# Optimization experiments

Measured on AMD Instinct MI355X. Metric: run time of the kernel, lower is better.

Reference implementation:

```python
import jax, jax.numpy as jnp
import numpy as np

C = 384      # c_s
NF = 16      # n_freq
H = 256      # mlp_hidden
B, K, N = 4, 2048, 16384
POS_WEIGHT = 1.5  # not used; see below


def _ln(x, g, b, eps=1e-5):
    m = x.mean(-1, keepdims=True)
    v = ((x - m) ** 2).mean(-1, keepdims=True)
    return (x - m) * jax.lax.rsqrt(v + eps) * g + b


def setup_inputs() -> dict:
    key = jax.random.key(0)
    ks = jax.random.split(key, 24)
    w = lambda k, shp: (jax.random.normal(k, shp, jnp.float32) * 0.02)
    inp = {
        "s_parent": jax.random.normal(ks[0], (B, K, C), jnp.float32),
        "mu_k": jax.random.normal(ks[1], (B, K, 3), jnp.float32),
        "R_k": jax.random.normal(ks[2], (B, K, 3, 3), jnp.float32),
        "s_k": jax.random.uniform(ks[3], (B, K, 3), jnp.float32),
        "a_idx": jax.random.randint(ks[4], (B, N), 0, K, jnp.int32),
        "node_mask": jnp.ones((B, N), jnp.float32),
        "pos01": jax.random.uniform(ks[5], (B, N), jnp.float32),
        # Pos01FourierEncoder: Linear(2*NF -> C)
        "pos_w": w(ks[6], (C, 2 * NF)), "pos_b": jnp.zeros((C,), jnp.float32),
        # q_proj: LayerNorm(C), Linear(C,C), SiLU, Linear(C,C)
        "q_ln_g": jnp.ones((C,), jnp.float32), "q_ln_b": jnp.zeros((C,), jnp.float32),
        "q_w1": w(ks[7], (C, C)), "q_b1": jnp.zeros((C,), jnp.float32),
        "q_w2": w(ks[8], (C, C)), "q_b2": jnp.zeros((C,), jnp.float32),
        # mlp: LayerNorm(C), Linear(C,H), SiLU, Linear(H,H), SiLU, Linear(H,3)
        "m_ln_g": jnp.ones((C,), jnp.float32), "m_ln_b": jnp.zeros((C,), jnp.float32),
        "m_w1": w(ks[9], (H, C)), "m_b1": jnp.zeros((H,), jnp.float32),
        "m_w2": w(ks[10], (H, H)), "m_b2": jnp.zeros((H,), jnp.float32),
        "m_w3": w(ks[11], (3, H)), "m_b3": jnp.zeros((3,), jnp.float32),
    }
    return inp


def reference(s_parent, mu_k, R_k, s_k, a_idx, node_mask, pos01,
              pos_w, pos_b, q_ln_g, q_ln_b, q_w1, q_b1, q_w2, q_b2,
              m_ln_g, m_ln_b, m_w1, m_b1, m_w2, m_b2, m_w3, m_b3):
    pos_weight = 1.0
    scale = 1.5
    mask = node_mask[..., None]  # [B,N,1]

    # Fourier positional encoding of pos01 in [0,1]
    freqs = (2.0 ** jnp.arange(NF, dtype=jnp.float32)) * np.float32(np.pi)
    ang = pos01[..., None] * freqs                          # [B,N,NF]
    feats = jnp.concatenate([jnp.sin(ang), jnp.cos(ang)], -1)  # [B,N,2NF]
    pos_emb = (feats @ pos_w.T + pos_b) * mask              # [B,N,C]

    idx = jnp.clip(a_idx, 0, K - 1)
    s_pi = jnp.take_along_axis(s_parent, idx[:, :, None], axis=1)  # [B,N,C]
    s_pi = s_pi + pos_weight * pos_emb

    # q_proj
    q = _ln(s_pi, q_ln_g, q_ln_b)
    q = jax.nn.silu(q @ q_w1.T + q_b1)
    q = (q @ q_w2.T + q_b2) * mask

    # mlp -> xi_hat
    h = _ln(q, m_ln_g, m_ln_b)
    h = jax.nn.silu(h @ m_w1.T + m_b1)
    h = jax.nn.silu(h @ m_w2.T + m_b2)
    xi = (h @ m_w3.T + m_b3) * mask
    xi_hat = jnp.tanh(xi) * scale                           # [B,N,3]

    # gather parent rigid params per node
    mu_i = jnp.take_along_axis(mu_k, idx[:, :, None], axis=1)            # [B,N,3]
    s_i = jnp.take_along_axis(jnp.maximum(s_k, 1e-8), idx[:, :, None], axis=1)
    R_i = jnp.take_along_axis(R_k, idx[:, :, None, None], axis=1)        # [B,N,3,3]

    # rigid apply: x = R @ (xi * s) + mu
    x_hat = jnp.einsum('bnij,bnj->bni', R_i, xi_hat * s_i) + mu_i
    x_hat = x_hat * mask
    return xi_hat, x_hat * 10.0, pos01
```

## Files before the change

kernel.cpp:

```cpp
#include <hip/hip_runtime.h>
#include <hip/hip_bf16.h>
#include <math.h>

#define C 384
#define NF 16
#define H 256
#define Bb 4
#define Kk 2048
#define Nn 16384
#define MB 64
#define LDA 392

typedef __attribute__((ext_vector_type(8))) short bf16x8;
typedef __attribute__((ext_vector_type(4))) float f32x4;
typedef __attribute__((ext_vector_type(4))) short s16x4;

#define POS_OFF 0
#define Q1_OFF  12288
#define Q2_OFF  159744
#define M1_OFF  307200
#define M2_OFF  405504
#define M3_OFF  471040
#define W_TOTAL 475136
#define NCONV   ((W_TOTAL + 255) / 256)
#define GQ_OFF 0
#define CQ_OFF 384
#define GM_OFF 768
#define CM_OFF 1024

#define BAR() __asm__ volatile("s_waitcnt lgkmcnt(0)\ns_barrier" ::: "memory")

__device__ __attribute__((always_inline)) inline short f2bf(float x) {
    return __builtin_bit_cast(short, __float2bfloat16(x));
}
__device__ __attribute__((always_inline)) inline float bf2f(short s) {
    return __bfloat162float(__builtin_bit_cast(__hip_bfloat16, s));
}
__device__ __attribute__((always_inline)) inline float silu(float v) {
    return v * __builtin_amdgcn_rcpf(1.f + __expf(-v));
}
__device__ __attribute__((always_inline)) inline s16x4 pack4(f32x4 v) {
    __hip_bfloat162 p0 = __float22bfloat162_rn(float2{v[0], v[1]});
    __hip_bfloat162 p1 = __float22bfloat162_rn(float2{v[2], v[3]});
    s16x4 o;
    o[0] = __builtin_bit_cast(short, p0.x);
    o[1] = __builtin_bit_cast(short, p0.y);
    o[2] = __builtin_bit_cast(short, p1.x);
    o[3] = __builtin_bit_cast(short, p1.y);
    return o;
}

__global__ __launch_bounds__(256) void prep(
    const float* __restrict__ pos_w, const float* __restrict__ q_w1,
    const float* __restrict__ q_w2,  const float* __restrict__ m_w1,
    const float* __restrict__ m_w2,  const float* __restrict__ m_w3,
    const float* __restrict__ q_ln_g, const float* __restrict__ q_ln_b,
    const float* __restrict__ m_ln_g, const float* __restrict__ m_ln_b,
    const float* __restrict__ q_b1,   const float* __restrict__ m_b1,
    short* __restrict__ ws, float* __restrict__ cst)
{
    __shared__ float rg[4], rc[4];
    int tid = threadIdx.x;
    int blk = blockIdx.x;
    if (blk < NCONV) {
        int i = blk * 256 + tid;
        if (i >= W_TOTAL) return;
        const float* src; int off, K;
        if      (i < Q1_OFF) { src = pos_w; off = POS_OFF; K = 32; }
        else if (i < Q2_OFF) { src = q_w1;  off = Q1_OFF;  K = 384; }
        else if (i < M1_OFF) { src = q_w2;  off = Q2_OFF;  K = 384; }
        else if (i < M2_OFF) { src = m_w1;  off = M1_OFF;  K = 384; }
        else if (i < M3_OFF) { src = m_w2;  off = M2_OFF;  K = 256; }
        else                 { src = m_w3;  off = M3_OFF;  K = 256; }
        int t = i - off;
        int chunk = t >> 9, r = t & 511;
        int ln = r >> 5, kq = r & 31;
        int NKm = K >> 5;
        int ntg = chunk / NKm, kk = chunk - ntg * NKm;
        int f = ntg * 16 + ln, k = kk * 32 + kq;
        float v;
        if (off == M3_OFF) v = (f < 3) ? m_w3[f * 256 + k] : 0.f;
        else               v = src[(size_t)f * K + k];
        if (off == Q1_OFF) v *= q_ln_g[k];
        if (off == M1_OFF) v *= m_ln_g[k];
        ws[i] = f2bf(v);
        return;
    }
    int f = blk - NCONV;
    const float *Wsrc, *lng, *lnb, *bias; int fr, go, co;
    if (f < 384) { Wsrc = q_w1; lng = q_ln_g; lnb = q_ln_b; bias = q_b1; fr = f;      go = GQ_OFF; co = CQ_OFF; }
    else         { Wsrc = m_w1; lng = m_ln_g; lnb = m_ln_b; bias = m_b1; fr = f - 384; go = GM_OFF; co = CM_OFF; }
    float g = 0.f, c = 0.f;
    for (int k = tid; k < 384; k += 256) {
        float wv = Wsrc[(size_t)fr * 384 + k];
        g += bf2f(f2bf(wv * lng[k]));
        c += wv * lnb[k];
    }
    #pragma unroll
    for (int d = 1; d < 64; d <<= 1) { g += __shfl_xor(g, d); c += __shfl_xor(c, d); }
    if ((tid & 63) == 0) { rg[tid >> 6] = g; rc[tid >> 6] = c; }
    __syncthreads();
    if (tid == 0) {
        cst[go + fr] = rg[0] + rg[1] + rg[2] + rg[3];
        cst[co + fr] = rc[0] + rc[1] + rc[2] + rc[3] + bias[fr];
    }
}

template<int K, int NT, int NTN, int KN, bool SILU_, bool MASK, bool LNIN, bool STATS>
__device__ __attribute__((always_inline)) inline void layer_ip(
    const short* __restrict__ W, const float* __restrict__ cb,
    const float* __restrict__ Gf, int FB,
    const short* __restrict__ Wn, int FBn,
    bf16x8 (&bin)[6],
    short (*__restrict__ xs)[LDA],
    float (*__restrict__ sc1)[4], float (*__restrict__ sc2)[4],
    const float* __restrict__ wmask, int w, int q, int ln)
{
    constexpr int NK = K / 32;
    const short* bp = W + (size_t)(FB / 16) * NK * 512 + ln * 32 + q * 8;

    f32x4 acc[4][NT];
    #pragma unroll
    for (int mt = 0; mt < 4; ++mt)
        #pragma unroll
        for (int nt = 0; nt < NT; ++nt)
            acc[mt][nt] = (f32x4){0.f, 0.f, 0.f, 0.f};

    bf16x8 Bbuf[3][NT];
    #pragma unroll
    for (int nt = 0; nt < NT; ++nt) Bbuf[0][nt] = bin[nt];
    #pragma unroll
    for (int nt = 0; nt < NT; ++nt)
        Bbuf[1][nt] = *(const bf16x8*)(bp + (size_t)nt * NK * 512 + 512);

    #pragma unroll
    for (int kc = 0; kc < NK; ++kc) {
        if (kc + 2 < NK) {
            #pragma unroll
            for (int nt = 0; nt < NT; ++nt)
                Bbuf[(kc + 2) % 3][nt] =
                    *(const bf16x8*)(bp + (size_t)nt * NK * 512 + (kc + 2) * 512);
        } else if (kc + 2 == NK) {
            #pragma unroll
            for (int nt = 0; nt < NTN; ++nt)
                bin[nt] = *(const bf16x8*)(Wn + ((size_t)(FBn / 16 + nt) * (KN / 32)) * 512 + ln * 32 + q * 8);
        }
        bf16x8 a[4];
        #pragma unroll
        for (int mt = 0; mt < 4; ++mt)
            a[mt] = *(const bf16x8*)&xs[mt * 16 + ln][kc * 32 + q * 8];
        #pragma unroll
        for (int nt = 0; nt < NT; ++nt)
            #pragma unroll
            for (int mt = 0; mt < 4; ++mt)
                acc[mt][nt] = __builtin_amdgcn_mfma_f32_16x16x32_bf16(
                    Bbuf[kc % 3][nt], a[mt], acc[mt][nt], 0, 0, 0);
    }

    BAR();

    float mk[4], rstd[4], rm[4];
    #pragma unroll
    for (int mt = 0; mt < 4; ++mt) {
        int m = mt * 16 + ln;
        if (MASK) mk[mt] = wmask[m];
        if (LNIN) {
            f32x4 p1 = *(const f32x4*)&sc1[m][0];
            f32x4 p2 = *(const f32x4*)&sc2[m][0];
            float t1 = p1[0] + p1[1] + p1[2] + p1[3];
            float t2 = p2[0] + p2[1] + p2[2] + p2[3];
            float mean = t1 * (1.f / 384.f);
            float var  = t2 * (1.f / 384.f) - mean * mean;
            rstd[mt] = rsqrtf(var + 1e-5f);
            rm[mt]   = rstd[mt] * mean;
        }
    }

    float s1[4] = {0.f,0.f,0.f,0.f}, s2[4] = {0.f,0.f,0.f,0.f};
    #pragma unroll
    for (int nt = 0; nt < NT; ++nt) {
        const int f0 = FB + nt * 16 + q * 4;
        f32x4 c4 = *(const f32x4*)&cb[f0];
        f32x4 g4;
        if (LNIN) g4 = *(const f32x4*)&Gf[f0];
        #pragma unroll
        for (int mt = 0; mt < 4; ++mt) {
            f32x4 vv;
            #pragma unroll
            for (int r = 0; r < 4; ++r) {
                float v;
                if (LNIN) v = fmaf(rstd[mt], acc[mt][nt][r], fmaf(-rm[mt], g4[r], c4[r]));
                else      v = acc[mt][nt][r] + c4[r];
                if (SILU_) v = silu(v);
                if (MASK) v *= mk[mt];
                if (STATS) { s1[mt] += v; s2[mt] += v * v; }
                vv[r] = v;
            }
            *(s16x4*)&xs[mt * 16 + ln][f0] = pack4(vv);
        }
    }
    if (STATS) {
        #pragma unroll
        for (int mt = 0; mt < 4; ++mt) {
            s1[mt] += __shfl_xor(s1[mt], 16); s2[mt] += __shfl_xor(s2[mt], 16);
            s1[mt] += __shfl_xor(s1[mt], 32); s2[mt] += __shfl_xor(s2[mt], 32);
        }
        if (q == 0) {
            #pragma unroll
            for (int mt = 0; mt < 4; ++mt) {
                sc1[mt * 16 + ln][w] = s1[mt];
                sc2[mt * 16 + ln][w] = s2[mt];
            }
        }
    }
    BAR();
}

__global__ __launch_bounds__(256, 2) void upxi64(
    const float* __restrict__ s_parent, const float* __restrict__ mu_k,
    const float* __restrict__ R_k,      const float* __restrict__ s_k,
    const int*   __restrict__ a_idx,    const float* __restrict__ node_mask,
    const float* __restrict__ pos01,
    const float* __restrict__ pos_b,
    const float* __restrict__ q_b2,     const float* __restrict__ m_b2,
    const float* __restrict__ m_b3,
    const short* __restrict__ wsb,      const float* __restrict__ cst,
    float* __restrict__ out)
{
    __shared__ short xs[MB][LDA];
    __shared__ float sc1[MB][4];
    __shared__ float sc2[MB][4];
    __shared__ float wmask[MB], wpos[MB];
    __shared__ int   widx[MB];

    const int tid  = threadIdx.x;
    const int w    = tid >> 6;
    const int lane = tid & 63;
    const int q    = lane >> 4;
    const int ln   = lane & 15;

    const int g0 = blockIdx.x * MB;
    const int b  = g0 / Nn;
    const int n0 = g0 % Nn;

    bf16x8 bin[6];
    #pragma unroll
    for (int nt = 0; nt < 6; ++nt)
        bin[nt] = *(const bf16x8*)(wsb + Q1_OFF + ((size_t)(w * 6 + nt) * 12) * 512 + ln * 32 + q * 8);

    if (tid < MB) {
        int gi = b * Nn + n0 + tid;
        int idx = a_idx[gi];
        widx[tid]  = min(max(idx, 0), Kk - 1);
        wmask[tid] = node_mask[gi];
        wpos[tid]  = pos01[gi];
    }
    BAR();

    const float* gbase = s_parent + (long)b * Kk * C;

    {
        const short* pos_wb = wsb + POS_OFF;
        const bool use_sin = (q < 2);
        const int kb = (q & 1) * 8;
        bf16x8 a[4];
        #pragma unroll
        for (int mt = 0; mt < 4; ++mt) {
            float p = wpos[mt * 16 + ln];
            #pragma unroll
            for (int e = 0; e < 8; ++e) {
                float fr = (float)(1 << (kb + e)) * 3.14159265358979323846f;
                float sv, cv;
                __sincosf(p * fr, &sv, &cv);
                a[mt][e] = f2bf(use_sin ? sv : cv);
            }
        }
        f32x4 acc[4][6];
        #pragma unroll
        for (int mt = 0; mt < 4; ++mt)
            #pragma unroll
            for (int nt = 0; nt < 6; ++nt)
                acc[mt][nt] = (f32x4){0.f, 0.f, 0.f, 0.f};
        #pragma unroll
        for (int nt = 0; nt < 6; ++nt) {
            bf16x8 bfr = *(const bf16x8*)&pos_wb[(w * 6 + nt) * 512 + ln * 32 + q * 8];
            #pragma unroll
            for (int mt = 0; mt < 4; ++mt)
                acc[mt][nt] = __builtin_amdgcn_mfma_f32_16x16x32_bf16(bfr, a[mt], acc[mt][nt], 0, 0, 0);
        }
        float mk[4]; int ix[4];
        #pragma unroll
        for (int mt = 0; mt < 4; ++mt) {
            mk[mt] = wmask[mt * 16 + ln];
            ix[mt] = widx[mt * 16 + ln];
        }
        float s1[4] = {0.f,0.f,0.f,0.f}, s2[4] = {0.f,0.f,0.f,0.f};
        #pragma unroll
        for (int nt = 0; nt < 6; ++nt) {
            const int f0 = w * 96 + nt * 16 + q * 4;
            f32x4 pb4 = *(const f32x4*)&pos_b[f0];
            #pragma unroll
            for (int mt = 0; mt < 4; ++mt) {
                f32x4 g4 = *(const f32x4*)&gbase[(long)ix[mt] * C + f0];
                f32x4 vv;
                #pragma unroll
                for (int r = 0; r < 4; ++r) {
                    float v = (acc[mt][nt][r] + pb4[r]) * mk[mt] + g4[r];
                    s1[mt] += v; s2[mt] += v * v;
                    vv[r] = v;
                }
                *(s16x4*)&xs[mt * 16 + ln][f0] = pack4(vv);
            }
        }
        #pragma unroll
        for (int mt = 0; mt < 4; ++mt) {
            s1[mt] += __shfl_xor(s1[mt], 16); s2[mt] += __shfl_xor(s2[mt], 16);
            s1[mt] += __shfl_xor(s1[mt], 32); s2[mt] += __shfl_xor(s2[mt], 32);
        }
        if (q == 0) {
            #pragma unroll
            for (int mt = 0; mt < 4; ++mt) {
                sc1[mt * 16 + ln][w] = s1[mt];
                sc2[mt * 16 + ln][w] = s2[mt];
            }
        }
    }
    BAR();

    layer_ip<384, 6, 6, 384, true,  false, true,  false>(wsb + Q1_OFF, cst + CQ_OFF,
        cst + GQ_OFF, w * 96, wsb + Q2_OFF, w * 96, bin, xs, sc1, sc2, wmask, w, q, ln);
    layer_ip<384, 6, 4, 384, false, true,  false, true >(wsb + Q2_OFF, q_b2,
        nullptr, w * 96, wsb + M1_OFF, w * 64, bin, xs, sc1, sc2, wmask, w, q, ln);
    layer_ip<384, 4, 4, 256, true,  false, true,  false>(wsb + M1_OFF, cst + CM_OFF,
        cst + GM_OFF, w * 64, wsb + M2_OFF, w * 64, bin, xs, sc1, sc2, wmask, w, q, ln);
    layer_ip<256, 4, 1, 256, true,  false, false, false>(wsb + M2_OFF, m_b2,
        nullptr, w * 64, wsb + M3_OFF, 0, bin, xs, sc1, sc2, wmask, w, q, ln);

    {
        const short* W3 = wsb + M3_OFF;
        f32x4 a3 = (f32x4){0.f, 0.f, 0.f, 0.f};
        #pragma unroll
        for (int kc = 0; kc < 8; ++kc) {
            bf16x8 a  = *(const bf16x8*)&xs[w * 16 + ln][kc * 32 + q * 8];
            bf16x8 bf = (kc == 0) ? bin[0]
                      : *(const bf16x8*)(W3 + kc * 512 + ln * 32 + q * 8);
            a3 = __builtin_amdgcn_mfma_f32_16x16x32_bf16(bf, a, a3, 0, 0, 0);
        }
        if (q == 0) {
            int m = w * 16 + ln;
            float mkv = wmask[m];
            #pragma unroll
            for (int r = 0; r < 3; ++r) {
                float v = (a3[r] + m_b3[r]) * mkv;
                sc1[m][r] = tanhf(v) * 1.5f;
            }
        }
    }

    if (lane < 16) {
        int m = w * 16 + lane;
        long gi = (long)b * Nn + n0 + m;
        long pk = (long)b * Kk + widx[m];
        float mkv = wmask[m];
        float xv[3], yv[3], xiv[3];
        #pragma unroll
        for (int j = 0; j < 3; ++j) {
            xiv[j] = sc1[m][j];
            float sc = fmaxf(s_k[pk * 3 + j], 1e-8f);
            xv[j] = xiv[j] * sc;
        }
        #pragma unroll
        for (int i = 0; i < 3; ++i) {
            float a = R_k[pk * 9 + i * 3 + 0] * xv[0]
                    + R_k[pk * 9 + i * 3 + 1] * xv[1]
                    + R_k[pk * 9 + i * 3 + 2] * xv[2]
                    + mu_k[pk * 3 + i];
            yv[i] = a * mkv * 10.f;
        }
        float* o0 = out;
        float* o1 = out + (long)Bb * Nn * 3;
        float* o2 = out + (long)Bb * Nn * 6;
        #pragma unroll
        for (int j = 0; j < 3; ++j) { o0[gi * 3 + j] = xiv[j]; o1[gi * 3 + j] = yv[j]; }
        o2[gi] = wpos[m];
    }
}

extern "C" void kernel_launch(void* const* d_in, const int* in_sizes, int n_in,
                              void* d_out, int out_size, void* d_ws, size_t ws_size,
                              hipStream_t stream) {
    const float* s_parent = (const float*)d_in[0];
    const float* mu_k     = (const float*)d_in[1];
    const float* R_k      = (const float*)d_in[2];
    const float* s_k      = (const float*)d_in[3];
    const int*   a_idx    = (const int*)  d_in[4];
    const float* node_mask= (const float*)d_in[5];
    const float* pos01    = (const float*)d_in[6];
    const float* pos_w    = (const float*)d_in[7];
    const float* pos_b    = (const float*)d_in[8];
    const float* q_ln_g   = (const float*)d_in[9];
    const float* q_ln_b   = (const float*)d_in[10];
    const float* q_w1     = (const float*)d_in[11];
    const float* q_b1     = (const float*)d_in[12];
    const float* q_w2     = (const float*)d_in[13];
    const float* q_b2     = (const float*)d_in[14];
    const float* m_ln_g   = (const float*)d_in[15];
    const float* m_ln_b   = (const float*)d_in[16];
    const float* m_w1     = (const float*)d_in[17];
    const float* m_b1     = (const float*)d_in[18];
    const float* m_w2     = (const float*)d_in[19];
    const float* m_b2     = (const float*)d_in[20];
    const float* m_w3     = (const float*)d_in[21];
    const float* m_b3     = (const float*)d_in[22];

    short* wsb = (short*)d_ws;
    float* cst = (float*)(wsb + W_TOTAL);

    prep<<<NCONV + 640, 256, 0, stream>>>(
        pos_w, q_w1, q_w2, m_w1, m_w2, m_w3,
        q_ln_g, q_ln_b, m_ln_g, m_ln_b, q_b1, m_b1, wsb, cst);

    int blocks = (Bb * Nn) / MB;
    upxi64<<<blocks, 256, 0, stream>>>(
        s_parent, mu_k, R_k, s_k, a_idx, node_mask, pos01,
        pos_b, q_b2, m_b2, m_b3, wsb, cst, (float*)d_out);
}
```

Measured before the change: 195.2 us.

## Reorder packed weights k-chunk-major and cut B prefetch depth to raise occupancy

The prep kernel now packs each weight matrix with the k-chunk index outermost and the feature tile innermost, so all tiles a wave needs for one k step sit next to each other. The MFMA layer loop drops its triple-buffered B registers for a single buffer that is reloaded after each step's MFMAs, and the next layer's first chunk is fetched after the loop. This frees registers so launch bounds can ask for 3 blocks per SIMD instead of 2. The cost is a shallower prefetch, which may expose global/L2 load latency on each k step unless the extra occupancy hides it.

```diff
diff --git a/kernel.cpp b/kernel.cpp
--- a/kernel.cpp
+++ b/kernel.cpp
@@ -65,19 +65,19 @@
     if (blk < NCONV) {
         int i = blk * 256 + tid;
         if (i >= W_TOTAL) return;
-        const float* src; int off, K;
-        if      (i < Q1_OFF) { src = pos_w; off = POS_OFF; K = 32; }
-        else if (i < Q2_OFF) { src = q_w1;  off = Q1_OFF;  K = 384; }
-        else if (i < M1_OFF) { src = q_w2;  off = Q2_OFF;  K = 384; }
-        else if (i < M2_OFF) { src = m_w1;  off = M1_OFF;  K = 384; }
-        else if (i < M3_OFF) { src = m_w2;  off = M2_OFF;  K = 256; }
-        else                 { src = m_w3;  off = M3_OFF;  K = 256; }
+        const float* src; int off, K, F;
+        if      (i < Q1_OFF) { src = pos_w; off = POS_OFF; K = 32;  F = 384; }
+        else if (i < Q2_OFF) { src = q_w1;  off = Q1_OFF;  K = 384; F = 384; }
+        else if (i < M1_OFF) { src = q_w2;  off = Q2_OFF;  K = 384; F = 384; }
+        else if (i < M2_OFF) { src = m_w1;  off = M1_OFF;  K = 384; F = 256; }
+        else if (i < M3_OFF) { src = m_w2;  off = M2_OFF;  K = 256; F = 256; }
+        else                 { src = m_w3;  off = M3_OFF;  K = 256; F = 16;  }
         int t = i - off;
         int chunk = t >> 9, r = t & 511;
         int ln = r >> 5, kq = r & 31;
-        int NKm = K >> 5;
-        int ntg = chunk / NKm, kk = chunk - ntg * NKm;
-        int f = ntg * 16 + ln, k = kk * 32 + kq;
+        int FT = F >> 4;
+        int kc = chunk / FT, nt = chunk - kc * FT;
+        int f = nt * 16 + ln, k = kc * 32 + kq;
         float v;
         if (off == M3_OFF) v = (f < 3) ? m_w3[f * 256 + k] : 0.f;
         else               v = src[(size_t)f * K + k];
@@ -106,7 +106,7 @@
     }
 }
 
-template<int K, int NT, int NTN, int KN, bool SILU_, bool MASK, bool LNIN, bool STATS>
+template<int K, int FT, int NT, int NTN, bool SILU_, bool MASK, bool LNIN, bool STATS>
 __device__ __attribute__((always_inline)) inline void layer_ip(
     const short* __restrict__ W, const float* __restrict__ cb,
     const float* __restrict__ Gf, int FB,
@@ -117,7 +117,8 @@
     const float* __restrict__ wmask, int w, int q, int ln)
 {
     constexpr int NK = K / 32;
-    const short* bp = W + (size_t)(FB / 16) * NK * 512 + ln * 32 + q * 8;
+    const int loff = ln * 32 + q * 8;
+    const short* bw = W + (size_t)(FB / 16) * 512 + loff;
 
     f32x4 acc[4][NT];
     #pragma unroll
@@ -126,25 +127,12 @@
         for (int nt = 0; nt < NT; ++nt)
             acc[mt][nt] = (f32x4){0.f, 0.f, 0.f, 0.f};
 
-    bf16x8 Bbuf[3][NT];
-    #pragma unroll
-    for (int nt = 0; nt < NT; ++nt) Bbuf[0][nt] = bin[nt];
-    #pragma unroll
-    for (int nt = 0; nt < NT; ++nt)
-        Bbuf[1][nt] = *(const bf16x8*)(bp + (size_t)nt * NK * 512 + 512);
+    bf16x8 B[NT];
+    #pragma unroll
+    for (int nt = 0; nt < NT; ++nt) B[nt] = bin[nt];
 
     #pragma unroll
     for (int kc = 0; kc < NK; ++kc) {
-        if (kc + 2 < NK) {
-            #pragma unroll
-            for (int nt = 0; nt < NT; ++nt)
-                Bbuf[(kc + 2) % 3][nt] =
-                    *(const bf16x8*)(bp + (size_t)nt * NK * 512 + (kc + 2) * 512);
-        } else if (kc + 2 == NK) {
-            #pragma unroll
-            for (int nt = 0; nt < NTN; ++nt)
-                bin[nt] = *(const bf16x8*)(Wn + ((size_t)(FBn / 16 + nt) * (KN / 32)) * 512 + ln * 32 + q * 8);
-        }
         bf16x8 a[4];
         #pragma unroll
         for (int mt = 0; mt < 4; ++mt)
@@ -154,7 +142,20 @@
             #pragma unroll
             for (int mt = 0; mt < 4; ++mt)
                 acc[mt][nt] = __builtin_amdgcn_mfma_f32_16x16x32_bf16(
-                    Bbuf[kc % 3][nt], a[mt], acc[mt][nt], 0, 0, 0);
+                    B[nt], a[mt], acc[mt][nt], 0, 0, 0);
+        if (kc + 1 < NK) {
+            const short* cb_ = bw + (size_t)(kc + 1) * FT * 512;
+            #pragma unroll
+            for (int nt = 0; nt < NT; ++nt)
+                B[nt] = *(const bf16x8*)(cb_ + nt * 512);
+        }
+    }
+
+    {
+        const short* nb = Wn + (size_t)(FBn / 16) * 512 + loff;
+        #pragma unroll
+        for (int nt = 0; nt < NTN; ++nt)
+            bin[nt] = *(const bf16x8*)(nb + nt * 512);
     }
 
     BAR();
@@ -216,7 +217,7 @@
     BAR();
 }
 
-__global__ __launch_bounds__(256, 2) void upxi64(
+__global__ __launch_bounds__(256, 3) void upxi64(
     const float* __restrict__ s_parent, const float* __restrict__ mu_k,
     const float* __restrict__ R_k,      const float* __restrict__ s_k,
     const int*   __restrict__ a_idx,    const float* __restrict__ node_mask,
@@ -244,9 +245,12 @@
     const int n0 = g0 % Nn;
 
     bf16x8 bin[6];
-    #pragma unroll
-    for (int nt = 0; nt < 6; ++nt)
-        bin[nt] = *(const bf16x8*)(wsb + Q1_OFF + ((size_t)(w * 6 + nt) * 12) * 512 + ln * 32 + q * 8);
+    {
+        const short* nb = wsb + Q1_OFF + (size_t)(w * 6) * 512 + ln * 32 + q * 8;
+        #pragma unroll
+        for (int nt = 0; nt < 6; ++nt)
+            bin[nt] = *(const bf16x8*)(nb + nt * 512);
+    }
 
     if (tid < MB) {
         int gi = b * Nn + n0 + tid;
@@ -327,13 +331,13 @@
     }
     BAR();
 
-    layer_ip<384, 6, 6, 384, true,  false, true,  false>(wsb + Q1_OFF, cst + CQ_OFF,
+    layer_ip<384, 24, 6, 6, true,  false, true,  false>(wsb + Q1_OFF, cst + CQ_OFF,
         cst + GQ_OFF, w * 96, wsb + Q2_OFF, w * 96, bin, xs, sc1, sc2, wmask, w, q, ln);
-    layer_ip<384, 6, 4, 384, false, true,  false, true >(wsb + Q2_OFF, q_b2,
+    layer_ip<384, 24, 6, 4, false, true,  false, true >(wsb + Q2_OFF, q_b2,
         nullptr, w * 96, wsb + M1_OFF, w * 64, bin, xs, sc1, sc2, wmask, w, q, ln);
-    layer_ip<384, 4, 4, 256, true,  false, true,  false>(wsb + M1_OFF, cst + CM_OFF,
+    layer_ip<384, 16, 4, 4, true,  false, true,  false>(wsb + M1_OFF, cst + CM_OFF,
         cst + GM_OFF, w * 64, wsb + M2_OFF, w * 64, bin, xs, sc1, sc2, wmask, w, q, ln);
-    layer_ip<256, 4, 1, 256, true,  false, false, false>(wsb + M2_OFF, m_b2,
+    layer_ip<256, 16, 4, 1, true,  false, false, false>(wsb + M2_OFF, m_b2,
         nullptr, w * 64, wsb + M3_OFF, 0, bin, xs, sc1, sc2, wmask, w, q, ln);
 
     {
```

Result: slower. 203.9 us (+4.5%).
